# Optimization experiments

Hardware: AMD Instinct MI355X
Metric: run time of the kernel (lower is better)

Reference implementation:

```python
import jax, jax.numpy as jnp
import numpy as np

D_MODEL = 2048
N_HEADS = 8
EXPAND_K = 1
EXPAND_V = 2
DK = D_MODEL * EXPAND_K // N_HEADS      # 256 per-head key dim
DV = D_MODEL * EXPAND_V // N_HEADS      # 512 per-head value dim
INTER = 5632
EPS = 1e-6
CHUNK = 64


def setup_inputs() -> dict:
    key = jax.random.key(0)
    ks = jax.random.split(key, 12)
    d = D_MODEL
    s = lambda fan_in: 1.0 / np.sqrt(fan_in)
    return {
        "hidden_states": jax.random.normal(ks[0], (2, 2048, d), jnp.float32),
        "attn_norm_w": jnp.ones((d,), jnp.float32),
        "q_w": jax.random.normal(ks[1], (d, d * EXPAND_K), jnp.float32) * s(d),
        "k_w": jax.random.normal(ks[2], (d, d * EXPAND_K), jnp.float32) * s(d),
        "v_w": jax.random.normal(ks[3], (d, d * EXPAND_V), jnp.float32) * s(d),
        "g_w": jax.random.normal(ks[4], (d, d * EXPAND_V), jnp.float32) * s(d),
        "o_w": jax.random.normal(ks[5], (d * EXPAND_V, d), jnp.float32) * s(d * EXPAND_V),
        "gnorm_w": jnp.ones((DV,), jnp.float32),
        "mlp_norm_w": jnp.ones((d,), jnp.float32),
        "gate_w": jax.random.normal(ks[6], (d, INTER * 2), jnp.float32) * s(d),
        "down_w": jax.random.normal(ks[7], (INTER, d), jnp.float32) * s(INTER),
    }


def rmsnorm(x, w, eps=EPS):
    return x * jax.lax.rsqrt(jnp.mean(x * x, axis=-1, keepdims=True) + eps) * w


def rope(x):
    # x: [B, T, H, D]; non-interleaved rotary on full head dim
    T, D = x.shape[1], x.shape[-1]
    inv_freq = 1.0 / (10000.0 ** (jnp.arange(0, D, 2, dtype=jnp.float32) / D))
    ang = jnp.arange(T, dtype=jnp.float32)[:, None] * inv_freq  # [T, D/2]
    cos = jnp.cos(ang)[None, :, None, :]
    sin = jnp.sin(ang)[None, :, None, :]
    x1, x2 = jnp.split(x, 2, axis=-1)
    return jnp.concatenate([x1 * cos - x2 * sin, x2 * cos + x1 * sin], axis=-1)


def chunk_retention(q, k, v):
    # q,k: [B,T,H,Dk], v: [B,T,H,Dv]; chunkwise-recurrent RetNet retention
    B, T, H, Dk = q.shape
    Dv = v.shape[-1]
    C = CHUNK
    N = T // C
    gamma = 1.0 - jnp.exp2(-5.0 - jnp.arange(H, dtype=jnp.float32))  # [H]
    i = jnp.arange(C, dtype=jnp.float32)
    diff = i[:, None] - i[None, :]
    Dmask = jnp.where(diff >= 0, gamma[:, None, None] ** diff, 0.0)   # [H,C,C]
    cross_decay = gamma[:, None] ** (i[None, :] + 1.0)                # [H,C]
    k_decay = gamma[:, None] ** (C - 1.0 - i[None, :])                # [H,C]
    chunk_decay = gamma ** C                                          # [H]

    # -> [N, B, H, C, D]
    to_chunks = lambda x: jnp.moveaxis(
        x.reshape(B, N, C, H, x.shape[-1]).transpose(0, 1, 3, 2, 4), 1, 0)
    qc, kc, vc = to_chunks(q), to_chunks(k), to_chunks(v)

    def body(S, inp):
        qb, kb, vb = inp  # [B,H,C,Dk/Dv]
        attn = jnp.einsum('bhid,bhjd->bhij', qb, kb) * Dmask
        o_intra = jnp.einsum('bhij,bhje->bhie', attn, vb)
        o_cross = jnp.einsum('bhid,bhde->bhie', qb * cross_decay[None, :, :, None], S)
        S = chunk_decay[None, :, None, None] * S + \
            jnp.einsum('bhid,bhie->bhde', kb * k_decay[None, :, :, None], vb)
        return S, o_intra + o_cross

    S0 = jnp.zeros((B, H, Dk, Dv), q.dtype)
    _, o = jax.lax.scan(body, S0, (qc, kc, vc))  # o: [N,B,H,C,Dv]
    return jnp.moveaxis(o, 0, 1).transpose(0, 1, 3, 2, 4).reshape(B, T, H, Dv)


def reference(hidden_states, attn_norm_w, q_w, k_w, v_w, g_w, o_w, gnorm_w,
              mlp_norm_w, gate_w, down_w):
    B, T, d = hidden_states.shape
    residual = hidden_states
    h = rmsnorm(hidden_states, attn_norm_w)

    # MultiScaleRetention
    q = (h @ q_w).reshape(B, T, N_HEADS, DK)
    k = (h @ k_w).reshape(B, T, N_HEADS, DK)
    v = (h @ v_w).reshape(B, T, N_HEADS, DV)
    g = (h @ g_w).reshape(B, T, N_HEADS, DV)
    q, k = rope(q), rope(k)
    q = q * (DK ** -0.5)
    o = chunk_retention(q, k, v)
    # fused RMSNorm + swish gate (per head over Dv)
    o = rmsnorm(o, gnorm_w) * (g * jax.nn.sigmoid(g))
    h = o.reshape(B, T, N_HEADS * DV) @ o_w

    # fused-residual RMSNorm
    residual = h + residual
    h = rmsnorm(residual, mlp_norm_w)

    # SwiGLU MLP
    y = h @ gate_w
    gate, y = jnp.split(y, 2, axis=-1)
    h = (gate * jax.nn.sigmoid(gate) * y) @ down_w
    return residual + h
```

## Files before the change

kernel.cpp:

```cpp
#include <hip/hip_runtime.h>
#include <cstdint>
#include <cstddef>

typedef unsigned short u16;
typedef __attribute__((ext_vector_type(4))) float f32x4;
typedef __attribute__((ext_vector_type(4))) unsigned int u32x4;

__device__ __forceinline__ float b2f(u16 u) {
  union { unsigned int i; float f; } x; x.i = ((unsigned int)u) << 16; return x.f;
}
__device__ __forceinline__ u16 f2b(float f) {
  union { float f; unsigned int i; } x; x.f = f;
  unsigned int i = x.i;
  i += 0x7fffu + ((i >> 16) & 1u);
  return (u16)(i >> 16);
}

__device__ __forceinline__ void mfma_bf16(f32x4& c, u32x4 a, u32x4 b) {
  asm("v_mfma_f32_16x16x32_bf16 %0, %1, %2, %0" : "+v"(c) : "v"(a), "v"(b));
}

__device__ __forceinline__ void async_ld16(const u16* g, u16* l) {
  typedef __attribute__((address_space(1))) const unsigned int GU;
  typedef __attribute__((address_space(3))) unsigned int LU;
  __builtin_amdgcn_global_load_lds((GU*)g, (LU*)l, 16, 0, 0);
}

__global__ __launch_bounds__(256)
void transpose_cast_kernel(const float* __restrict__ in, u16* __restrict__ out,
                           int K, int N, int ldin) {
  __shared__ float tile[64][65];
  const int nb = N >> 6;
  const int bk = blockIdx.x / nb, bn = blockIdx.x % nb;
  const int k0 = bk * 64, n0 = bn * 64;
  const int tid = threadIdx.x;
#pragma unroll
  for (int p = 0; p < 16; ++p) {
    int idx = p * 256 + tid;
    int r = idx >> 6, c = idx & 63;
    tile[r][c] = in[(size_t)(k0 + r) * ldin + n0 + c];
  }
  __syncthreads();
#pragma unroll
  for (int p = 0; p < 16; ++p) {
    int idx = p * 256 + tid;
    int r = idx >> 6, c = idx & 63;
    out[(size_t)(n0 + r) * K + k0 + c] = f2b(tile[c][r]);
  }
}

__global__ __launch_bounds__(256)
void rmsnorm_cast_kernel(const float* __restrict__ x, const float* __restrict__ w,
                         u16* __restrict__ out) {
  const int row = blockIdx.x, tid = threadIdx.x;
  const float* xr = x + (size_t)row * 2048;
  float4 a = ((const float4*)xr)[tid * 2];
  float4 b = ((const float4*)xr)[tid * 2 + 1];
  float ss = a.x*a.x + a.y*a.y + a.z*a.z + a.w*a.w
           + b.x*b.x + b.y*b.y + b.z*b.z + b.w*b.w;
#pragma unroll
  for (int m = 32; m; m >>= 1) ss += __shfl_xor(ss, m);
  __shared__ float ps[4];
  if ((tid & 63) == 0) ps[tid >> 6] = ss;
  __syncthreads();
  const float sc = rsqrtf((ps[0] + ps[1] + ps[2] + ps[3]) * (1.0f / 2048.0f) + 1e-6f);
  const int base = tid * 8;
  const float vals[8] = {a.x, a.y, a.z, a.w, b.x, b.y, b.z, b.w};
  union { u16 h[8]; uint4 v4[2]; } o;
#pragma unroll
  for (int j = 0; j < 8; ++j) o.h[j] = f2b(vals[j] * sc * w[base + j]);
  *(uint4*)&out[(size_t)row * 2048 + base] = o.v4[0];
  *(uint4*)&out[(size_t)row * 2048 + base + 8] = o.v4[1];
}

__global__ __launch_bounds__(256)
void rmsnorm_bf16_kernel(const u16* __restrict__ x, const float* __restrict__ w,
                         u16* __restrict__ out) {
  const int row = blockIdx.x, tid = threadIdx.x;
  union { uint4 v4; u16 h[8]; } p;
  p.v4 = *(const uint4*)&x[(size_t)row * 2048 + tid * 8];
  float v[8];
  float ss = 0.f;
#pragma unroll
  for (int j = 0; j < 8; ++j) { v[j] = b2f(p.h[j]); ss += v[j] * v[j]; }
#pragma unroll
  for (int m = 32; m; m >>= 1) ss += __shfl_xor(ss, m);
  __shared__ float ps[4];
  if ((tid & 63) == 0) ps[tid >> 6] = ss;
  __syncthreads();
  const float sc = rsqrtf((ps[0] + ps[1] + ps[2] + ps[3]) * (1.0f / 2048.0f) + 1e-6f);
  union { u16 h[8]; uint4 v4; } o;
#pragma unroll
  for (int j = 0; j < 8; ++j) o.h[j] = f2b(v[j] * sc * w[tid * 8 + j]);
  *(uint4*)&out[(size_t)row * 2048 + tid * 8] = o.v4;
}

__global__ __launch_bounds__(256)
void rope_table_kernel(float* __restrict__ ct, float* __restrict__ st) {
  const int idx = blockIdx.x * 256 + threadIdx.x;
  const int t = idx >> 7, i = idx & 127;
  const float e = -(float)i * (0.0078125f * log2f(10000.0f));
  const float ang = (float)t * exp2f(e);
  ct[idx] = cosf(ang);
  st[idx] = sinf(ang);
}

__global__ __launch_bounds__(256)
void rope_apply_kernel(u16* __restrict__ x, const float* __restrict__ ct,
                       const float* __restrict__ st, float scale) {
  const int gid = blockIdx.x * 256 + threadIdx.x;
  const int r = gid >> 8;
  const int rem = gid & 255;
  const int h = rem >> 5;
  const int i4 = (rem & 31) * 4;
  const int t = r & 2047;
  const size_t o1 = (size_t)r * 2048 + h * 256 + i4;
  union { ushort4 v; u16 h4[4]; } p1, p2, q1, q2;
  p1.v = *(ushort4*)&x[o1];
  p2.v = *(ushort4*)&x[o1 + 128];
  const float4 c = *(const float4*)&ct[t * 128 + i4];
  const float4 s = *(const float4*)&st[t * 128 + i4];
  const float cc[4] = {c.x, c.y, c.z, c.w};
  const float sn[4] = {s.x, s.y, s.z, s.w};
#pragma unroll
  for (int j = 0; j < 4; ++j) {
    float x1 = b2f(p1.h4[j]), x2 = b2f(p2.h4[j]);
    q1.h4[j] = f2b((x1 * cc[j] - x2 * sn[j]) * scale);
    q2.h4[j] = f2b((x2 * cc[j] + x1 * sn[j]) * scale);
  }
  *(ushort4*)&x[o1] = q1.v;
  *(ushort4*)&x[o1 + 128] = q2.v;
}

template <int EPI>
__global__ __launch_bounds__(256, 2)
void gemm_bt(const u16* __restrict__ A, const u16* __restrict__ Bt,
             void* Cout, const float* fsrc, const u16* hsrc, int N, int K) {
  __shared__ __align__(16) u16 As[128 * 32];
  __shared__ __align__(16) u16 Bs[128 * 32];
  const int tid = threadIdx.x;
  const int l = tid & 63, w = tid >> 6;
  const int lr = l & 15, hi = l >> 4;
  const int nbn = N >> 7;
  const int bm = blockIdx.x / nbn, bn = blockIdx.x % nbn;
  const int f0 = w * 512 + l * 8;
  const int r0 = f0 >> 5, c0 = f0 & 31;
  const u16* ga0 = A + (size_t)(bm * 128 + r0) * K + c0;
  const u16* ga1 = ga0 + (size_t)64 * K;
  const u16* gb0 = Bt + (size_t)(bn * 128 + r0) * K + c0;
  const u16* gb1 = gb0 + (size_t)64 * K;
  u16* la = As + w * 512;
  u16* lb = Bs + w * 512;
  f32x4 acc[4][4];
#pragma unroll
  for (int m = 0; m < 4; ++m)
#pragma unroll
    for (int n = 0; n < 4; ++n) acc[m][n] = (f32x4){0.f, 0.f, 0.f, 0.f};
  const int wr = (w >> 1) * 64, wc = (w & 1) * 64;
  for (int k0 = 0; k0 < K; k0 += 32) {
    async_ld16(ga0 + k0, la);
    async_ld16(ga1 + k0, la + 2048);
    async_ld16(gb0 + k0, lb);
    async_ld16(gb1 + k0, lb + 2048);
    __syncthreads();
    u32x4 af[4], bfr[4];
#pragma unroll
    for (int m = 0; m < 4; ++m)
      af[m] = *(const u32x4*)&As[(wr + m * 16 + lr) * 32 + hi * 8];
#pragma unroll
    for (int n = 0; n < 4; ++n)
      bfr[n] = *(const u32x4*)&Bs[(wc + n * 16 + lr) * 32 + hi * 8];
#pragma unroll
    for (int m = 0; m < 4; ++m)
#pragma unroll
      for (int n = 0; n < 4; ++n) mfma_bf16(acc[m][n], af[m], bfr[n]);
    __syncthreads();
  }
  const size_t crow0 = (size_t)(bm * 128 + wr);
  const int ccol0 = bn * 128 + wc;
#pragma unroll
  for (int m = 0; m < 4; ++m)
#pragma unroll
    for (int n = 0; n < 4; ++n)
#pragma unroll
      for (int j = 0; j < 4; ++j) {
        size_t r = crow0 + m * 16 + hi * 4 + j;
        size_t c = (size_t)(ccol0 + n * 16 + lr);
        size_t idx = r * N + c;
        float a = acc[m][n][j];
        if (EPI == 1) {
          ((u16*)Cout)[idx] = f2b(a);
        } else if (EPI == 2) {
          ((float*)Cout)[idx] = a + b2f(hsrc[idx]);
        } else if (EPI == 3) {
          float u = b2f(hsrc[idx]);
          ((u16*)Cout)[idx] = f2b(a / (1.0f + expf(-a)) * u);
        } else {
          ((u16*)Cout)[idx] = f2b(a + fsrc[idx]);
        }
      }
}

#define LGQ 264
#define LGV 72
__global__ __launch_bounds__(256)
void retention_kernel(const u16* __restrict__ q, const u16* __restrict__ k,
                      const u16* __restrict__ v, u16* __restrict__ o) {
  __shared__ __align__(16) u16 qs[64 * LGQ];
  __shared__ __align__(16) u16 ks[64 * LGQ];
  __shared__ __align__(16) u16 stb[64 * LGQ];
  __shared__ __align__(16) u16 ktd[256 * LGV];
  __shared__ __align__(16) u16 vts[64 * LGV];
  __shared__ __align__(16) u16 ab[64 * LGV];

  const int tid = threadIdx.x;
  const int l = tid & 63, w = tid >> 6;
  const int lr = l & 15, hi = l >> 4;
  const int bid = blockIdx.x;
  const int sl = bid & 7;
  const int hh = (bid >> 3) & 7;
  const int b = bid >> 6;
  const float gamma = 1.0f - exp2f(-5.0f - (float)hh);
  const float lg = log2f(gamma);
  const float cdk = exp2f(64.0f * lg);
  const int e0 = sl * 64;
  const float kd = exp2f((float)(63 - (tid >> 2)) * lg);

  f32x4 st[16];
#pragma unroll
  for (int t = 0; t < 16; ++t) st[t] = (f32x4){0.f, 0.f, 0.f, 0.f};

  for (int n = 0; n < 32; ++n) {
    const int row0 = b * 2048 + n * 64;
#pragma unroll
    for (int t = 0; t < 16; ++t)
#pragma unroll
      for (int j = 0; j < 4; ++j)
        stb[(w * 16 + hi * 4 + j) * LGQ + t * 16 + lr] = f2b(st[t][j]);
#pragma unroll
    for (int p = 0; p < 8; ++p) {
      int idx = p * 256 + tid;
      int c = idx >> 5, s = (idx & 31) * 8;
      *(uint4*)&qs[c * LGQ + s] =
          *(const uint4*)&q[(size_t)(row0 + c) * 2048 + hh * 256 + s];
      *(uint4*)&ks[c * LGQ + s] =
          *(const uint4*)&k[(size_t)(row0 + c) * 2048 + hh * 256 + s];
    }
    {
      int e = tid & 63, cq = tid >> 6;
#pragma unroll
      for (int cc = 0; cc < 16; ++cc) {
        int c = cq * 16 + cc;
        vts[e * LGV + c] = v[(size_t)(row0 + c) * 4096 + hh * 512 + e0 + e];
      }
    }
    {
      int c = tid >> 2, dq = (tid & 3) * 64;
      const u16* krow = k + (size_t)(row0 + c) * 2048 + hh * 256 + dq;
#pragma unroll
      for (int d8 = 0; d8 < 8; ++d8) {
        union { uint4 v4; u16 h[8]; } pk;
        pk.v4 = *(const uint4*)(krow + d8 * 8);
#pragma unroll
        for (int j = 0; j < 8; ++j)
          ktd[(dq + d8 * 8 + j) * LGV + c] = f2b(b2f(pk.h[j]) * kd);
      }
    }
    __syncthreads();

    f32x4 att[4];
#pragma unroll
    for (int jf = 0; jf < 4; ++jf) att[jf] = (f32x4){0.f, 0.f, 0.f, 0.f};
#pragma unroll
    for (int kk = 0; kk < 8; ++kk) {
      u32x4 a = *(const u32x4*)&qs[(w * 16 + lr) * LGQ + kk * 32 + hi * 8];
#pragma unroll
      for (int jf = 0; jf < 4; ++jf) {
        u32x4 bb = *(const u32x4*)&ks[(jf * 16 + lr) * LGQ + kk * 32 + hi * 8];
        mfma_bf16(att[jf], a, bb);
      }
    }
#pragma unroll
    for (int jf = 0; jf < 4; ++jf)
#pragma unroll
      for (int j = 0; j < 4; ++j) {
        int i = w * 16 + hi * 4 + j;
        int jc = jf * 16 + lr;
        float mv = (i >= jc) ? exp2f((float)(i - jc) * lg) : 0.0f;
        ab[i * LGV + jc] = f2b(att[jf][j] * mv);
      }
    __syncthreads();

    f32x4 occ[4];
#pragma unroll
    for (int ef = 0; ef < 4; ++ef) occ[ef] = (f32x4){0.f, 0.f, 0.f, 0.f};
#pragma unroll
    for (int kk = 0; kk < 8; ++kk) {
      u32x4 a = *(const u32x4*)&qs[(w * 16 + lr) * LGQ + kk * 32 + hi * 8];
#pragma unroll
      for (int ef = 0; ef < 4; ++ef) {
        u32x4 bb = *(const u32x4*)&stb[(ef * 16 + lr) * LGQ + kk * 32 + hi * 8];
        mfma_bf16(occ[ef], a, bb);
      }
    }
#pragma unroll
    for (int ef = 0; ef < 4; ++ef)
#pragma unroll
      for (int j = 0; j < 4; ++j) {
        int i = w * 16 + hi * 4 + j;
        occ[ef][j] *= exp2f((float)(i + 1) * lg);
      }
#pragma unroll
    for (int kk = 0; kk < 2; ++kk) {
      u32x4 a = *(const u32x4*)&ab[(w * 16 + lr) * LGV + kk * 32 + hi * 8];
#pragma unroll
      for (int ef = 0; ef < 4; ++ef) {
        u32x4 bb = *(const u32x4*)&vts[(ef * 16 + lr) * LGV + kk * 32 + hi * 8];
        mfma_bf16(occ[ef], a, bb);
      }
    }
#pragma unroll
    for (int ef = 0; ef < 4; ++ef)
#pragma unroll
      for (int j = 0; j < 4; ++j) {
        int i = w * 16 + hi * 4 + j;
        o[(size_t)(row0 + i) * 4096 + hh * 512 + e0 + ef * 16 + lr] = f2b(occ[ef][j]);
      }
#pragma unroll
    for (int t = 0; t < 16; ++t) {
      st[t][0] *= cdk; st[t][1] *= cdk; st[t][2] *= cdk; st[t][3] *= cdk;
    }
#pragma unroll
    for (int kk = 0; kk < 2; ++kk) {
      u32x4 a = *(const u32x4*)&vts[(w * 16 + lr) * LGV + kk * 32 + hi * 8];
#pragma unroll
      for (int t = 0; t < 16; ++t) {
        u32x4 bb = *(const u32x4*)&ktd[(t * 16 + lr) * LGV + kk * 32 + hi * 8];
        mfma_bf16(st[t], a, bb);
      }
    }
    __syncthreads();
  }
}

__global__ __launch_bounds__(64)
void gating_kernel(u16* __restrict__ o, const u16* __restrict__ g,
                   const float* __restrict__ gnw) {
  const int blk = blockIdx.x;
  const size_t base = (size_t)blk * 512;
  const int l = threadIdx.x;
  union { uint4 v4; u16 h[8]; } ov, gv;
  ov.v4 = *(const uint4*)&o[base + l * 8];
  float x[8];
  float ss = 0.f;
#pragma unroll
  for (int j = 0; j < 8; ++j) { x[j] = b2f(ov.h[j]); ss += x[j] * x[j]; }
#pragma unroll
  for (int m = 32; m; m >>= 1) ss += __shfl_xor(ss, m);
  const float sc = rsqrtf(ss * (1.0f / 512.0f) + 1e-6f);
  gv.v4 = *(const uint4*)&g[base + l * 8];
  union { u16 h[8]; uint4 v4; } ou;
#pragma unroll
  for (int j = 0; j < 8; ++j) {
    float gvf = b2f(gv.h[j]);
    float sig = 1.0f / (1.0f + expf(-gvf));
    ou.h[j] = f2b(x[j] * sc * gnw[l * 8 + j] * gvf * sig);
  }
  *(uint4*)&o[base + l * 8] = ou.v4;
}

extern "C" void kernel_launch(void* const* d_in, const int* in_sizes, int n_in,
                              void* d_out, int out_size, void* d_ws, size_t ws_size,
                              hipStream_t stream) {
  (void)in_sizes; (void)n_in; (void)out_size; (void)ws_size;
  const float* hidden      = (const float*)d_in[0];
  const float* attn_norm_w = (const float*)d_in[1];
  const float* q_w         = (const float*)d_in[2];
  const float* k_w         = (const float*)d_in[3];
  const float* v_w         = (const float*)d_in[4];
  const float* g_w         = (const float*)d_in[5];
  const float* o_w         = (const float*)d_in[6];
  const float* gnorm_w     = (const float*)d_in[7];
  const float* mlp_norm_w  = (const float*)d_in[8];
  const float* gate_w      = (const float*)d_in[9];
  const float* down_w      = (const float*)d_in[10];
  float* outp = (float*)d_out;

  char* ws = (char*)d_ws;
  size_t off = 0;
  auto alloc = [&](size_t bytes) -> char* {
    char* p = ws + off;
    off += (bytes + 255) & ~(size_t)255;
    return p;
  };
  u16*   W    = (u16*)alloc(23068672ULL);
  float* ctab = (float*)alloc(1048576ULL);
  float* stab = (float*)alloc(1048576ULL);
  u16*   hb   = (u16*)alloc(16777216ULL);
  u16*   qb   = (u16*)alloc(16777216ULL);
  u16*   kb   = (u16*)alloc(16777216ULL);
  u16*   vb   = (u16*)alloc(33554432ULL);
  u16*   gb   = (u16*)alloc(33554432ULL);
  u16*   ob   = (u16*)alloc(33554432ULL);
  u16*   resb = (u16*)alloc(16777216ULL);
  u16*   ybU  = vb;

  rope_table_kernel<<<1024, 256, 0, stream>>>(ctab, stab);
  rmsnorm_cast_kernel<<<4096, 256, 0, stream>>>(hidden, attn_norm_w, hb);

  transpose_cast_kernel<<<1024, 256, 0, stream>>>(q_w, W, 2048, 2048, 2048);
  gemm_bt<1><<<512, 256, 0, stream>>>(hb, W, (void*)qb, nullptr, nullptr, 2048, 2048);
  transpose_cast_kernel<<<1024, 256, 0, stream>>>(k_w, W, 2048, 2048, 2048);
  gemm_bt<1><<<512, 256, 0, stream>>>(hb, W, (void*)kb, nullptr, nullptr, 2048, 2048);
  transpose_cast_kernel<<<2048, 256, 0, stream>>>(v_w, W, 2048, 4096, 4096);
  gemm_bt<1><<<1024, 256, 0, stream>>>(hb, W, (void*)vb, nullptr, nullptr, 4096, 2048);
  transpose_cast_kernel<<<2048, 256, 0, stream>>>(g_w, W, 2048, 4096, 4096);
  gemm_bt<1><<<1024, 256, 0, stream>>>(hb, W, (void*)gb, nullptr, nullptr, 4096, 2048);

  rope_apply_kernel<<<4096, 256, 0, stream>>>(qb, ctab, stab, 0.0625f);
  rope_apply_kernel<<<4096, 256, 0, stream>>>(kb, ctab, stab, 1.0f);

  retention_kernel<<<128, 256, 0, stream>>>(qb, kb, vb, ob);

  gating_kernel<<<32768, 64, 0, stream>>>(ob, gb, gnorm_w);

  transpose_cast_kernel<<<2048, 256, 0, stream>>>(o_w, W, 4096, 2048, 2048);
  gemm_bt<4><<<512, 256, 0, stream>>>(ob, W, (void*)resb, hidden, nullptr, 2048, 4096);

  rmsnorm_bf16_kernel<<<4096, 256, 0, stream>>>(resb, mlp_norm_w, hb);

  transpose_cast_kernel<<<2816, 256, 0, stream>>>(gate_w + 5632, W, 2048, 5632, 11264);
  gemm_bt<1><<<1408, 256, 0, stream>>>(hb, W, (void*)ybU, nullptr, nullptr, 5632, 2048);
  transpose_cast_kernel<<<2816, 256, 0, stream>>>(gate_w, W, 2048, 5632, 11264);
  gemm_bt<3><<<1408, 256, 0, stream>>>(hb, W, (void*)ybU, nullptr, ybU, 5632, 2048);

  transpose_cast_kernel<<<2816, 256, 0, stream>>>(down_w, W, 5632, 2048, 2048);
  gemm_bt<2><<<512, 256, 0, stream>>>(ybU, W, (void*)outp, nullptr, resb, 2048, 5632);
}
```

Measured before the change: 1.098 ms.

## Split retention over more blocks and waves, pretranspose K globally

After: 1.040 ms. -5.3%, faster.

```diff
diff --git a/kernel.cpp b/kernel.cpp
--- a/kernel.cpp
+++ b/kernel.cpp
@@ -46,6 +46,33 @@
     int idx = p * 256 + tid;
     int r = idx >> 6, c = idx & 63;
     out[(size_t)(n0 + r) * K + k0 + c] = f2b(tile[c][r]);
+  }
+}
+
+__global__ __launch_bounds__(256)
+void transpose_k_kernel(const u16* __restrict__ kb, u16* __restrict__ kt) {
+  __shared__ u16 tile[64][72];
+  const int bid = blockIdx.x;
+  const int dd = bid & 3, tt = (bid >> 2) & 31;
+  const int h = (bid >> 7) & 7, b = bid >> 10;
+  const int t0 = tt * 64, d0 = dd * 64;
+  const int tid = threadIdx.x;
+#pragma unroll
+  for (int p = 0; p < 2; ++p) {
+    int idx = p * 256 + tid;
+    int r = idx >> 3, cq = (idx & 7) * 8;
+    *(uint4*)&tile[r][cq] =
+        *(const uint4*)&kb[(size_t)(b * 2048 + t0 + r) * 2048 + h * 256 + d0 + cq];
+  }
+  __syncthreads();
+#pragma unroll
+  for (int p = 0; p < 2; ++p) {
+    int idx = p * 256 + tid;
+    int r = idx >> 3, cq = (idx & 7) * 8;
+    union { u16 h8[8]; uint4 v4; } o;
+#pragma unroll
+    for (int j = 0; j < 8; ++j) o.h8[j] = tile[cq + j][r];
+    *(uint4*)&kt[((size_t)(b * 8 + h) * 256 + d0 + r) * 2048 + t0 + cq] = o.v4;
   }
 }
 
@@ -201,142 +228,134 @@
       }
 }
 
-#define LGQ 264
-#define LGV 72
-__global__ __launch_bounds__(256)
+#define LGK 264
+#define LGC 72
+__global__ __launch_bounds__(512)
 void retention_kernel(const u16* __restrict__ q, const u16* __restrict__ k,
-                      const u16* __restrict__ v, u16* __restrict__ o) {
-  __shared__ __align__(16) u16 qs[64 * LGQ];
-  __shared__ __align__(16) u16 ks[64 * LGQ];
-  __shared__ __align__(16) u16 stb[64 * LGQ];
-  __shared__ __align__(16) u16 ktd[256 * LGV];
-  __shared__ __align__(16) u16 vts[64 * LGV];
-  __shared__ __align__(16) u16 ab[64 * LGV];
+                      const u16* __restrict__ kt, const u16* __restrict__ v,
+                      u16* __restrict__ o) {
+  __shared__ __align__(16) u16 ks[64 * LGK];
+  __shared__ __align__(16) u16 stb[32 * LGK];
+  __shared__ __align__(16) u16 ktd[256 * LGC];
+  __shared__ __align__(16) u16 vts[32 * LGC];
+  __shared__ __align__(16) u16 ab[64 * LGC];
+  __shared__ float kdt[64];
 
   const int tid = threadIdx.x;
   const int l = tid & 63, w = tid >> 6;
   const int lr = l & 15, hi = l >> 4;
+  const int wr = w >> 1;
+  const int eb = w & 1;
   const int bid = blockIdx.x;
-  const int sl = bid & 7;
-  const int hh = (bid >> 3) & 7;
-  const int b = bid >> 6;
+  const int sl = bid & 15;
+  const int hh = (bid >> 4) & 7;
+  const int b = bid >> 7;
   const float gamma = 1.0f - exp2f(-5.0f - (float)hh);
   const float lg = log2f(gamma);
   const float cdk = exp2f(64.0f * lg);
-  const int e0 = sl * 64;
-  const float kd = exp2f((float)(63 - (tid >> 2)) * lg);
-
-  f32x4 st[16];
-#pragma unroll
-  for (int t = 0; t < 16; ++t) st[t] = (f32x4){0.f, 0.f, 0.f, 0.f};
+  const int e0 = sl * 32;
+
+  if (tid < 64) kdt[tid] = exp2f((float)(63 - tid) * lg);
+  __syncthreads();
+
+  f32x4 st[4];
+#pragma unroll
+  for (int t = 0; t < 4; ++t) st[t] = (f32x4){0.f, 0.f, 0.f, 0.f};
 
   for (int n = 0; n < 32; ++n) {
     const int row0 = b * 2048 + n * 64;
-#pragma unroll
-    for (int t = 0; t < 16; ++t)
+    const int t0 = n * 64;
+#pragma unroll
+    for (int t = 0; t < 4; ++t)
 #pragma unroll
       for (int j = 0; j < 4; ++j)
-        stb[(w * 16 + hi * 4 + j) * LGQ + t * 16 + lr] = f2b(st[t][j]);
-#pragma unroll
-    for (int p = 0; p < 8; ++p) {
-      int idx = p * 256 + tid;
+        stb[(eb * 16 + hi * 4 + j) * LGK + (wr * 4 + t) * 16 + lr] = f2b(st[t][j]);
+    u32x4 qf[8];
+#pragma unroll
+    for (int kk = 0; kk < 8; ++kk)
+      qf[kk] = *(const u32x4*)&q[(size_t)(row0 + wr * 16 + lr) * 2048 +
+                                 hh * 256 + kk * 32 + hi * 8];
+#pragma unroll
+    for (int p = 0; p < 4; ++p) {
+      int idx = p * 512 + tid;
       int c = idx >> 5, s = (idx & 31) * 8;
-      *(uint4*)&qs[c * LGQ + s] =
-          *(const uint4*)&q[(size_t)(row0 + c) * 2048 + hh * 256 + s];
-      *(uint4*)&ks[c * LGQ + s] =
+      *(uint4*)&ks[c * LGK + s] =
           *(const uint4*)&k[(size_t)(row0 + c) * 2048 + hh * 256 + s];
     }
-    {
-      int e = tid & 63, cq = tid >> 6;
-#pragma unroll
-      for (int cc = 0; cc < 16; ++cc) {
-        int c = cq * 16 + cc;
-        vts[e * LGV + c] = v[(size_t)(row0 + c) * 4096 + hh * 512 + e0 + e];
+#pragma unroll
+    for (int p = 0; p < 4; ++p) {
+      int idx = p * 512 + tid;
+      int d = idx >> 3, cq = (idx & 7) * 8;
+      union { uint4 v4; u16 h[8]; } pk;
+      pk.v4 = *(const uint4*)&kt[((size_t)(b * 8 + hh) * 256 + d) * 2048 + t0 + cq];
+      union { u16 h[8]; uint4 v4; } wo;
+#pragma unroll
+      for (int j2 = 0; j2 < 8; ++j2)
+        wo.h[j2] = f2b(b2f(pk.h[j2]) * kdt[cq + j2]);
+      *(uint4*)&ktd[d * LGC + cq] = wo.v4;
+    }
+#pragma unroll
+    for (int p = 0; p < 4; ++p) {
+      int c = (tid >> 5) + p * 16, e = tid & 31;
+      vts[e * LGC + c] = v[(size_t)(row0 + c) * 4096 + hh * 512 + e0 + e];
+    }
+    __syncthreads();
+
+    f32x4 att[2];
+    att[0] = (f32x4){0.f, 0.f, 0.f, 0.f};
+    att[1] = (f32x4){0.f, 0.f, 0.f, 0.f};
+#pragma unroll
+    for (int kk = 0; kk < 8; ++kk) {
+#pragma unroll
+      for (int jf = 0; jf < 2; ++jf) {
+        u32x4 bb = *(const u32x4*)&ks[(eb * 32 + jf * 16 + lr) * LGK + kk * 32 + hi * 8];
+        mfma_bf16(att[jf], qf[kk], bb);
       }
     }
-    {
-      int c = tid >> 2, dq = (tid & 3) * 64;
-      const u16* krow = k + (size_t)(row0 + c) * 2048 + hh * 256 + dq;
-#pragma unroll
-      for (int d8 = 0; d8 < 8; ++d8) {
-        union { uint4 v4; u16 h[8]; } pk;
-        pk.v4 = *(const uint4*)(krow + d8 * 8);
-#pragma unroll
-        for (int j = 0; j < 8; ++j)
-          ktd[(dq + d8 * 8 + j) * LGV + c] = f2b(b2f(pk.h[j]) * kd);
+#pragma unroll
+    for (int jf = 0; jf < 2; ++jf)
+#pragma unroll
+      for (int j = 0; j < 4; ++j) {
+        int i = wr * 16 + hi * 4 + j;
+        int jc = eb * 32 + jf * 16 + lr;
+        float mv = (i >= jc) ? exp2f((float)(i - jc) * lg) : 0.0f;
+        ab[i * LGC + jc] = f2b(att[jf][j] * mv);
       }
+    f32x4 occ = (f32x4){0.f, 0.f, 0.f, 0.f};
+#pragma unroll
+    for (int kk = 0; kk < 8; ++kk) {
+      u32x4 bb = *(const u32x4*)&stb[(eb * 16 + lr) * LGK + kk * 32 + hi * 8];
+      mfma_bf16(occ, qf[kk], bb);
     }
     __syncthreads();
 
-    f32x4 att[4];
-#pragma unroll
-    for (int jf = 0; jf < 4; ++jf) att[jf] = (f32x4){0.f, 0.f, 0.f, 0.f};
-#pragma unroll
-    for (int kk = 0; kk < 8; ++kk) {
-      u32x4 a = *(const u32x4*)&qs[(w * 16 + lr) * LGQ + kk * 32 + hi * 8];
-#pragma unroll
-      for (int jf = 0; jf < 4; ++jf) {
-        u32x4 bb = *(const u32x4*)&ks[(jf * 16 + lr) * LGQ + kk * 32 + hi * 8];
-        mfma_bf16(att[jf], a, bb);
-      }
-    }
-#pragma unroll
-    for (int jf = 0; jf < 4; ++jf)
-#pragma unroll
-      for (int j = 0; j < 4; ++j) {
-        int i = w * 16 + hi * 4 + j;
-        int jc = jf * 16 + lr;
-        float mv = (i >= jc) ? exp2f((float)(i - jc) * lg) : 0.0f;
-        ab[i * LGV + jc] = f2b(att[jf][j] * mv);
-      }
-    __syncthreads();
-
-    f32x4 occ[4];
-#pragma unroll
-    for (int ef = 0; ef < 4; ++ef) occ[ef] = (f32x4){0.f, 0.f, 0.f, 0.f};
-#pragma unroll
-    for (int kk = 0; kk < 8; ++kk) {
-      u32x4 a = *(const u32x4*)&qs[(w * 16 + lr) * LGQ + kk * 32 + hi * 8];
-#pragma unroll
-      for (int ef = 0; ef < 4; ++ef) {
-        u32x4 bb = *(const u32x4*)&stb[(ef * 16 + lr) * LGQ + kk * 32 + hi * 8];
-        mfma_bf16(occ[ef], a, bb);
-      }
-    }
-#pragma unroll
-    for (int ef = 0; ef < 4; ++ef)
-#pragma unroll
-      for (int j = 0; j < 4; ++j) {
-        int i = w * 16 + hi * 4 + j;
-        occ[ef][j] *= exp2f((float)(i + 1) * lg);
-      }
+#pragma unroll
+    for (int j = 0; j < 4; ++j) {
+      int i = wr * 16 + hi * 4 + j;
+      occ[j] *= exp2f((float)(i + 1) * lg);
+    }
 #pragma unroll
     for (int kk = 0; kk < 2; ++kk) {
-      u32x4 a = *(const u32x4*)&ab[(w * 16 + lr) * LGV + kk * 32 + hi * 8];
-#pragma unroll
-      for (int ef = 0; ef < 4; ++ef) {
-        u32x4 bb = *(const u32x4*)&vts[(ef * 16 + lr) * LGV + kk * 32 + hi * 8];
-        mfma_bf16(occ[ef], a, bb);
-      }
-    }
-#pragma unroll
-    for (int ef = 0; ef < 4; ++ef)
-#pragma unroll
-      for (int j = 0; j < 4; ++j) {
-        int i = w * 16 + hi * 4 + j;
-        o[(size_t)(row0 + i) * 4096 + hh * 512 + e0 + ef * 16 + lr] = f2b(occ[ef][j]);
-      }
-#pragma unroll
-    for (int t = 0; t < 16; ++t) {
+      u32x4 aa = *(const u32x4*)&ab[(wr * 16 + lr) * LGC + kk * 32 + hi * 8];
+      u32x4 bb = *(const u32x4*)&vts[(eb * 16 + lr) * LGC + kk * 32 + hi * 8];
+      mfma_bf16(occ, aa, bb);
+    }
+#pragma unroll
+    for (int j = 0; j < 4; ++j) {
+      int i = wr * 16 + hi * 4 + j;
+      o[(size_t)(row0 + i) * 4096 + hh * 512 + e0 + eb * 16 + lr] = f2b(occ[j]);
+    }
+#pragma unroll
+    for (int t = 0; t < 4; ++t) {
       st[t][0] *= cdk; st[t][1] *= cdk; st[t][2] *= cdk; st[t][3] *= cdk;
     }
 #pragma unroll
     for (int kk = 0; kk < 2; ++kk) {
-      u32x4 a = *(const u32x4*)&vts[(w * 16 + lr) * LGV + kk * 32 + hi * 8];
-#pragma unroll
-      for (int t = 0; t < 16; ++t) {
-        u32x4 bb = *(const u32x4*)&ktd[(t * 16 + lr) * LGV + kk * 32 + hi * 8];
-        mfma_bf16(st[t], a, bb);
+      u32x4 aa = *(const u32x4*)&vts[(eb * 16 + lr) * LGC + kk * 32 + hi * 8];
+#pragma unroll
+      for (int t = 0; t < 4; ++t) {
+        u32x4 bb = *(const u32x4*)&ktd[((wr * 4 + t) * 16 + lr) * LGC + kk * 32 + hi * 8];
+        mfma_bf16(st[t], aa, bb);
       }
     }
     __syncthreads();
@@ -404,6 +423,7 @@
   u16*   ob   = (u16*)alloc(33554432ULL);
   u16*   resb = (u16*)alloc(16777216ULL);
   u16*   ybU  = vb;
+  u16*   kt   = W;
 
   rope_table_kernel<<<1024, 256, 0, stream>>>(ctab, stab);
   rmsnorm_cast_kernel<<<4096, 256, 0, stream>>>(hidden, attn_norm_w, hb);
@@ -419,8 +439,9 @@
 
   rope_apply_kernel<<<4096, 256, 0, stream>>>(qb, ctab, stab, 0.0625f);
   rope_apply_kernel<<<4096, 256, 0, stream>>>(kb, ctab, stab, 1.0f);
-
-  retention_kernel<<<128, 256, 0, stream>>>(qb, kb, vb, ob);
+  transpose_k_kernel<<<2048, 256, 0, stream>>>(kb, kt);
+
+  retention_kernel<<<256, 512, 0, stream>>>(qb, kb, kt, vb, ob);
 
   gating_kernel<<<32768, 64, 0, stream>>>(ob, gb, gnorm_w);
 
```
